# Kernel optimization log

Hardware: AMD Instinct MI355X
Metric: run time of the kernel (lower is better)

## Reference

```python
import jax, jax.numpy as jnp
import numpy as np

N, E, F_IN, HID, EPS = 50000, 800000, 128, 256, 1e-5

def _glorot(key, shape):
    scale = 1.0 / np.sqrt(shape[0])
    return jax.random.uniform(key, shape, jnp.float32, -scale, scale)

def setup_inputs() -> dict:
    key = jax.random.key(0)
    ks = jax.random.split(key, 20)
    x = jax.random.normal(ks[0], (N, F_IN), jnp.float32)
    edge_index = jax.random.randint(ks[1], (2, E), 0, N, jnp.int64)
    inp = {"x": x, "edge_index": edge_index}
    dims = [F_IN, HID, HID]
    for i in range(3):
        d_in = dims[i]
        inp[f"Wn{i}"] = _glorot(ks[2 + 4 * i], (d_in, HID))      # lin_l weight (neighbors), with bias
        inp[f"bn{i}"] = jnp.zeros((HID,), jnp.float32)
        inp[f"Wr{i}"] = _glorot(ks[3 + 4 * i], (d_in, HID))      # lin_r weight (root), no bias
        inp[f"g{i}"] = jnp.ones((HID,), jnp.float32)              # BN gamma
        inp[f"b{i}"] = jnp.zeros((HID,), jnp.float32)             # BN beta
    return inp

def _sage_bn_elu(x, src, dst, Wn, bn, Wr, g, b):
    # mean aggregation of source features onto destination nodes
    agg = jax.ops.segment_sum(x[src], dst, num_segments=N)                      # [N, d_in]
    deg = jax.ops.segment_sum(jnp.ones((src.shape[0],), x.dtype), dst, num_segments=N)
    agg = agg / jnp.maximum(deg, 1.0)[:, None]
    h = agg @ Wn + bn + x @ Wr                                                  # SAGEConv(root_weight=True)
    mu = jnp.mean(h, axis=0)
    var = jnp.mean((h - mu) ** 2, axis=0)                                       # biased var (BN training)
    h = (h - mu) * jax.lax.rsqrt(var + EPS) * g + b
    return jnp.where(h > 0, h, jnp.expm1(h))                                    # ELU(alpha=1)

def reference(x, edge_index, Wn0, bn0, Wr0, g0, b0, Wn1, bn1, Wr1, g1, b1, Wn2, bn2, Wr2, g2, b2):
    src, dst = edge_index[0], edge_index[1]
    h = _sage_bn_elu(x, src, dst, Wn0, bn0, Wr0, g0, b0)
    h = _sage_bn_elu(h, src, dst, Wn1, bn1, Wr1, g1, b1)
    h = _sage_bn_elu(h, src, dst, Wn2, bn2, Wr2, g2, b2)
    return h
```

## Files before the change

### kernel.cpp

```cpp
#include <hip/hip_runtime.h>
#include <math.h>

#define N_NODES 50000
#define N_EDGES 800000
#define F_IN    128
#define HID     256
#define BN_EPS  1e-5f
#define SCAN_BLOCKS ((N_NODES + 255) / 256)
#define RB256       ((N_NODES + 255) / 256)

typedef unsigned int uint;
typedef __attribute__((ext_vector_type(8))) short bf16x8;
typedef __attribute__((ext_vector_type(4))) float f32x4;

__device__ __forceinline__ float bf2f(unsigned short u) {
    return __uint_as_float((uint)u << 16);
}
__device__ __forceinline__ unsigned short f2bf(float f) {
    uint u = __float_as_uint(f);
    return (unsigned short)((u + 0x7FFFu + ((u >> 16) & 1u)) >> 16);
}

__device__ __forceinline__ void gload16(const unsigned short* g, unsigned short* l) {
    __builtin_amdgcn_global_load_lds(
        (const __attribute__((address_space(1))) void*)g,
        (__attribute__((address_space(3))) void*)l, 16, 0, 0);
}

__device__ __forceinline__ void acc_u4(float* a, uint4 v) {
    a[0] += bf2f((unsigned short)(v.x & 0xFFFF)); a[1] += bf2f((unsigned short)(v.x >> 16));
    a[2] += bf2f((unsigned short)(v.y & 0xFFFF)); a[3] += bf2f((unsigned short)(v.y >> 16));
    a[4] += bf2f((unsigned short)(v.z & 0xFFFF)); a[5] += bf2f((unsigned short)(v.z >> 16));
    a[6] += bf2f((unsigned short)(v.w & 0xFFFF)); a[7] += bf2f((unsigned short)(v.w >> 16));
}
__device__ __forceinline__ void acc_u4m(float* a, uint4 v, float m) {
    a[0] += m * bf2f((unsigned short)(v.x & 0xFFFF)); a[1] += m * bf2f((unsigned short)(v.x >> 16));
    a[2] += m * bf2f((unsigned short)(v.y & 0xFFFF)); a[3] += m * bf2f((unsigned short)(v.y >> 16));
    a[4] += m * bf2f((unsigned short)(v.z & 0xFFFF)); a[5] += m * bf2f((unsigned short)(v.z >> 16));
    a[6] += m * bf2f((unsigned short)(v.w & 0xFFFF)); a[7] += m * bf2f((unsigned short)(v.w >> 16));
}

__global__ void hist_kernel(const int* __restrict__ dst, int* __restrict__ deg) {
    int e = blockIdx.x * blockDim.x + threadIdx.x;
    if (e < N_EDGES) atomicAdd(&deg[dst[e]], 1);
}

__global__ __launch_bounds__(256) void scan1_kernel(const int* __restrict__ deg,
                                                    int* __restrict__ row_ptr,
                                                    int* __restrict__ partials) {
    __shared__ int sm[256];
    int i = blockIdx.x * 256 + threadIdx.x;
    int v = (i < N_NODES) ? deg[i] : 0;
    sm[threadIdx.x] = v;
    __syncthreads();
    for (int off = 1; off < 256; off <<= 1) {
        int t = (threadIdx.x >= off) ? sm[threadIdx.x - off] : 0;
        __syncthreads();
        sm[threadIdx.x] += t;
        __syncthreads();
    }
    if (i < N_NODES) row_ptr[i] = sm[threadIdx.x] - v;
    if (threadIdx.x == 255) partials[blockIdx.x] = sm[255];
}

__global__ __launch_bounds__(256) void scan2_kernel(int* __restrict__ partials) {
    __shared__ int sm[256];
    int t = threadIdx.x;
    int v = (t < SCAN_BLOCKS) ? partials[t] : 0;
    sm[t] = v;
    __syncthreads();
    for (int off = 1; off < 256; off <<= 1) {
        int p = (t >= off) ? sm[t - off] : 0;
        __syncthreads();
        sm[t] += p;
        __syncthreads();
    }
    if (t < SCAN_BLOCKS) partials[t] = sm[t] - v;
}

__global__ __launch_bounds__(256) void scan3_kernel(int* __restrict__ row_ptr,
                                                    int* __restrict__ cursor,
                                                    const int* __restrict__ partials) {
    int i = blockIdx.x * 256 + threadIdx.x;
    if (i < N_NODES) {
        int v = row_ptr[i] + partials[blockIdx.x];
        row_ptr[i] = v;
        cursor[i]  = v;
    }
    if (i == 0) row_ptr[N_NODES] = N_EDGES;
}

__global__ void fill_kernel(const int* __restrict__ src, const int* __restrict__ dst,
                            int* __restrict__ cursor, int* __restrict__ csr_src) {
    int e = blockIdx.x * blockDim.x + threadIdx.x;
    if (e >= N_EDGES) return;
    int pos = atomicAdd(&cursor[dst[e]], 1);
    csr_src[pos] = src[e];
}

__global__ void cast_bf16_kernel(const float* __restrict__ x, unsigned short* __restrict__ xb,
                                 int total4) {
    int i = blockIdx.x * blockDim.x + threadIdx.x;
    if (i >= total4) return;
    float4 v = *(const float4*)&x[(long)i * 4];
    unsigned short o[4] = {f2bf(v.x), f2bf(v.y), f2bf(v.z), f2bf(v.w)};
    *(uint2*)&xb[(long)i * 4] = *(const uint2*)o;
}

__global__ __launch_bounds__(256) void wt_kernel(const float* __restrict__ Wn,
                                                 const float* __restrict__ Wr,
                                                 int K1, int KT, unsigned short* __restrict__ WT) {
    int n  = threadIdx.x;
    int k0 = blockIdx.x * 16;
    unsigned short o[16];
#pragma unroll
    for (int j = 0; j < 16; ++j) {
        int k = k0 + j;
        float v = (k < K1) ? Wn[k * HID + n] : Wr[(k - K1) * HID + n];
        o[j] = f2bf(v);
    }
    *(uint4*)&WT[(long)n * KT + k0]     = *(const uint4*)&o[0];
    *(uint4*)&WT[(long)n * KT + k0 + 8] = *(const uint4*)&o[8];
}

template<int D>
__global__ __launch_bounds__(256) void gather_mean_kernel(
    const unsigned short* __restrict__ x, const int* __restrict__ row_ptr,
    const int* __restrict__ csr_src, unsigned short* __restrict__ agg) {
    int node = blockIdx.x * 4 + (threadIdx.x >> 6);
    int lane = threadIdx.x & 63;
    if (node >= N_NODES) return;
    int beg = row_ptr[node], end = row_ptr[node + 1];
    float acc[8];
#pragma unroll
    for (int j = 0; j < 8; j++) acc[j] = 0.f;
    int e = beg;

    if constexpr (D == 256) {
        const int half = lane >> 5;
        const long lo  = (long)(lane & 31) * 8;
        for (; e + 8 <= end; e += 8) {
            int s0 = csr_src[e + half],     s1 = csr_src[e + 2 + half];
            int s2 = csr_src[e + 4 + half], s3 = csr_src[e + 6 + half];
            uint4 v0 = *(const uint4*)&x[(long)s0 * 256 + lo];
            uint4 v1 = *(const uint4*)&x[(long)s1 * 256 + lo];
            uint4 v2 = *(const uint4*)&x[(long)s2 * 256 + lo];
            uint4 v3 = *(const uint4*)&x[(long)s3 * 256 + lo];
            acc_u4(acc, v0); acc_u4(acc, v1); acc_u4(acc, v2); acc_u4(acc, v3);
        }
        for (; e + 2 <= end; e += 2) {
            int s0 = csr_src[e + half];
            uint4 v0 = *(const uint4*)&x[(long)s0 * 256 + lo];
            acc_u4(acc, v0);
        }
        if (e < end) {
            int s0 = csr_src[e];
            uint4 v0 = *(const uint4*)&x[(long)s0 * 256 + lo];
            acc_u4m(acc, v0, (half == 0) ? 1.f : 0.f);
        }
#pragma unroll
        for (int j = 0; j < 8; j++) acc[j] += __shfl_xor(acc[j], 32);
        float inv = 1.0f / fmaxf((float)(end - beg), 1.0f);
        if (half == 0) {
            unsigned short ov[8];
#pragma unroll
            for (int j = 0; j < 8; j++) ov[j] = f2bf(acc[j] * inv);
            *(uint4*)&agg[(long)node * 256 + lo] = *(const uint4*)ov;
        }
    } else {
        const int grp = lane >> 4;
        const long lo = (long)(lane & 15) * 8;
        for (; e + 8 <= end; e += 8) {
            int sA = csr_src[e + grp], sB = csr_src[e + 4 + grp];
            uint4 vA = *(const uint4*)&x[(long)sA * 128 + lo];
            uint4 vB = *(const uint4*)&x[(long)sB * 128 + lo];
            acc_u4(acc, vA); acc_u4(acc, vB);
        }
        for (; e + 4 <= end; e += 4) {
            int sA = csr_src[e + grp];
            uint4 vA = *(const uint4*)&x[(long)sA * 128 + lo];
            acc_u4(acc, vA);
        }
        for (; e < end; e++) {
            int s0 = csr_src[e];
            uint4 v0 = *(const uint4*)&x[(long)s0 * 128 + lo];
            acc_u4m(acc, v0, (grp == 0) ? 1.f : 0.f);
        }
#pragma unroll
        for (int j = 0; j < 8; j++) {
            acc[j] += __shfl_xor(acc[j], 32);
            acc[j] += __shfl_xor(acc[j], 16);
        }
        float inv = 1.0f / fmaxf((float)(end - beg), 1.0f);
        if (lane < 16) {
            unsigned short ov[8];
#pragma unroll
            for (int j = 0; j < 8; j++) ov[j] = f2bf(acc[j] * inv);
            *(uint4*)&agg[(long)node * 128 + lo] = *(const uint4*)ov;
        }
    }
}

template<int K1, int K2>
__global__ __launch_bounds__(512) void mfma_gemm_kernel(
    const unsigned short* __restrict__ A1, const unsigned short* __restrict__ A2,
    const unsigned short* __restrict__ WT, const float* __restrict__ bias,
    unsigned short* __restrict__ Hout, float* __restrict__ sred) {
    constexpr int KT = K1 + K2;
    constexpr int NITER = KT / 64;
    __shared__ unsigned short As[2][256 * 64];
    __shared__ unsigned short Bs[2][256 * 64];

    const int tid  = threadIdx.x;
    const int wave = tid >> 6;
    const int lane = tid & 63;
    const int m16  = lane & 15;
    const int quad = lane >> 4;
    const int WR   = wave >> 2;
    const int WC   = wave & 3;
    const int r0   = blockIdx.x * 256;
    const int rl = lane >> 3;
    const int cl = lane & 7;
    const int csw = cl ^ rl;

    f32x4 acc[8][4];
#pragma unroll
    for (int mt = 0; mt < 8; mt++)
#pragma unroll
        for (int nt = 0; nt < 4; nt++) acc[mt][nt] = (f32x4){0.f, 0.f, 0.f, 0.f};

    auto issue = [&](int t) {
        const int buf = t & 1;
        const int k0  = t * 64;
        const unsigned short* Ab;
        int pitch, kk;
        if (k0 < K1) { Ab = A1; pitch = K1; kk = k0; }
        else         { Ab = A2; pitch = K2; kk = k0 - K1; }
#pragma unroll
        for (int j = 0; j < 4; ++j) {
            int lr = wave * 32 + j * 8 + rl;
            long gr = min(r0 + lr, N_NODES - 1);
            gload16(&Ab[gr * pitch + kk + csw * 8], &As[buf][(wave * 32 + j * 8) * 64]);
        }
#pragma unroll
        for (int j = 0; j < 4; ++j) {
            long gn = wave * 32 + j * 8 + rl;
            gload16(&WT[gn * KT + k0 + csw * 8], &Bs[buf][(wave * 32 + j * 8) * 64]);
        }
    };

    issue(0);

#pragma unroll
    for (int it = 0; it < NITER; ++it) {
        const int cur = it & 1;
        if (it + 1 < NITER) {
            issue(it + 1);
            asm volatile("s_waitcnt vmcnt(8)" ::: "memory");
        } else {
            asm volatile("s_waitcnt vmcnt(0)" ::: "memory");
        }
        __builtin_amdgcn_s_barrier();
#pragma unroll
        for (int ks = 0; ks < 2; ++ks) {
            bf16x8 afrag[8], bfrag[4];
#pragma unroll
            for (int mt = 0; mt < 8; mt++) {
                int ar = WR * 128 + mt * 16 + m16;
                afrag[mt] = *(const bf16x8*)&As[cur][ar * 64 + (((ks * 4 + quad) ^ (m16 & 7)) * 8)];
            }
#pragma unroll
            for (int nt = 0; nt < 4; nt++) {
                int br = WC * 64 + nt * 16 + m16;
                bfrag[nt] = *(const bf16x8*)&Bs[cur][br * 64 + (((ks * 4 + quad) ^ (m16 & 7)) * 8)];
            }
#pragma unroll
            for (int mt = 0; mt < 8; mt++)
#pragma unroll
                for (int nt = 0; nt < 4; nt++)
                    acc[mt][nt] = __builtin_amdgcn_mfma_f32_16x16x32_bf16(
                        afrag[mt], bfrag[nt], acc[mt][nt], 0, 0, 0);
        }
        __builtin_amdgcn_s_barrier();
    }

#pragma unroll
    for (int nt = 0; nt < 4; nt++) {
        int lcol = WC * 64 + nt * 16 + m16;
        float bv = bias[lcol];
        float s = 0.f, q = 0.f;
#pragma unroll
        for (int mt = 0; mt < 8; mt++) {
#pragma unroll
            for (int reg = 0; reg < 4; reg++) {
                int row = r0 + WR * 128 + mt * 16 + quad * 4 + reg;
                float v = acc[mt][nt][reg] + bv;
                if (row < N_NODES) {
                    Hout[(long)row * HID + lcol] = f2bf(v);
                    s += v;
                    q += v * v;
                }
            }
        }
        s += __shfl_xor(s, 16); s += __shfl_xor(s, 32);
        q += __shfl_xor(q, 16); q += __shfl_xor(q, 32);
        if (quad == 0) {
            float* base = &sred[(long)(blockIdx.x * 2 + WR) * 512];
            base[lcol]       = s;
            base[256 + lcol] = q;
        }
    }
}

__global__ __launch_bounds__(512) void bn_reduce_kernel(const float* __restrict__ sred,
                                                        const float* __restrict__ g,
                                                        const float* __restrict__ b,
                                                        float* __restrict__ ss, int nrows) {
    __shared__ float qsm[256];
    int t  = threadIdx.x;
    int ch = t & 255;
    int off = (t < 256) ? 0 : 256;
    float S0 = 0.f, S1 = 0.f, S2 = 0.f, S3 = 0.f;
    int rb = 0;
    for (; rb + 4 <= nrows; rb += 4) {
        S0 += sred[(long)(rb + 0) * 512 + off + ch];
        S1 += sred[(long)(rb + 1) * 512 + off + ch];
        S2 += sred[(long)(rb + 2) * 512 + off + ch];
        S3 += sred[(long)(rb + 3) * 512 + off + ch];
    }
    for (; rb < nrows; rb++) S0 += sred[(long)rb * 512 + off + ch];
    float Sv = (S0 + S1) + (S2 + S3);
    if (t >= 256) qsm[ch] = Sv;
    __syncthreads();
    if (t < 256) {
        float mu  = Sv * (1.0f / N_NODES);
        float var = qsm[ch] * (1.0f / N_NODES) - mu * mu;
        var = fmaxf(var, 0.f);
        float sc = rsqrtf(var + BN_EPS) * g[ch];
        ss[ch]       = sc;
        ss[HID + ch] = b[ch] - mu * sc;
    }
}

template<bool OUT32>
__global__ void bn_elu_kernel(const unsigned short* __restrict__ h, const float* __restrict__ ss,
                              void* __restrict__ out) {
    const int total4 = N_NODES * HID / 4;
    int i = blockIdx.x * blockDim.x + threadIdx.x;
    if (i >= total4) return;
    int c4 = (i % (HID / 4)) * 4;
    uint2 v = *(const uint2*)&h[(long)i * 4];
    float4 sc = *(const float4*)&ss[c4];
    float4 sh = *(const float4*)&ss[HID + c4];
    float in[4] = {bf2f((unsigned short)(v.x & 0xFFFF)), bf2f((unsigned short)(v.x >> 16)),
                   bf2f((unsigned short)(v.y & 0xFFFF)), bf2f((unsigned short)(v.y >> 16))};
    float scv[4] = {sc.x, sc.y, sc.z, sc.w};
    float shv[4] = {sh.x, sh.y, sh.z, sh.w};
    float o[4];
#pragma unroll
    for (int j = 0; j < 4; j++) {
        float t = fmaf(in[j], scv[j], shv[j]);
        o[j] = t > 0.f ? t : expm1f(t);
    }
    if (OUT32) {
        float4 ov = {o[0], o[1], o[2], o[3]};
        *(float4*)&((float*)out)[(long)i * 4] = ov;
    } else {
        unsigned short ov[4] = {f2bf(o[0]), f2bf(o[1]), f2bf(o[2]), f2bf(o[3])};
        *(uint2*)&((unsigned short*)out)[(long)i * 4] = *(const uint2*)ov;
    }
}

extern "C" void kernel_launch(void* const* d_in, const int* in_sizes, int n_in,
                              void* d_out, int out_size, void* d_ws, size_t ws_size,
                              hipStream_t stream) {
    const float* x   = (const float*)d_in[0];
    const int*   ei  = (const int*)d_in[1];
    const int*   src = ei;
    const int*   dst = ei + N_EDGES;
    const float* Wn[3] = {(const float*)d_in[2],  (const float*)d_in[7],  (const float*)d_in[12]};
    const float* bn[3] = {(const float*)d_in[3],  (const float*)d_in[8],  (const float*)d_in[13]};
    const float* Wr[3] = {(const float*)d_in[4],  (const float*)d_in[9],  (const float*)d_in[14]};
    const float* g [3] = {(const float*)d_in[5],  (const float*)d_in[10], (const float*)d_in[15]};
    const float* b [3] = {(const float*)d_in[6],  (const float*)d_in[11], (const float*)d_in[16]};
    float* out = (float*)d_out;

    const size_t BF = (size_t)N_NODES * HID * 2;
    char* ws = (char*)d_ws;
    unsigned short* B0  = (unsigned short*)(ws);
    unsigned short* B1  = (unsigned short*)(ws + BF);
    unsigned short* B2  = (unsigned short*)(ws + 2 * BF);
    unsigned short* XB  = (unsigned short*)(ws + 3 * BF);
    char* ws2 = ws + 3 * BF + (size_t)N_NODES * F_IN * 2;
    unsigned short* WT0 = (unsigned short*)(ws2);
    unsigned short* WT1 = (unsigned short*)(ws2 + 256 * 256 * 2);
    unsigned short* WT2 = (unsigned short*)(ws2 + 256 * 256 * 2 + 256 * 512 * 2);
    char* ws3 = ws2 + 256 * 256 * 2 + 2 * (256 * 512 * 2);
    int*   row_ptr = (int*)ws3;
    int*   cursor  = row_ptr + (N_NODES + 1);
    int*   deg_i   = cursor + N_NODES;
    int*   partial = deg_i + N_NODES;
    int*   csr_src = partial + SCAN_BLOCKS;
    float* sred    = (float*)(csr_src + N_EDGES);
    float* ss      = sred + (size_t)2 * RB256 * 512;

    const int eb = (N_EDGES + 255) / 256;
    const int gather_blocks = (N_NODES + 3) / 4;
    const int elu_blocks = (N_NODES * HID / 4 + 255) / 256;

    hipMemsetAsync(deg_i, 0, N_NODES * sizeof(int), stream);
    hist_kernel<<<eb, 256, 0, stream>>>(dst, deg_i);
    scan1_kernel<<<SCAN_BLOCKS, 256, 0, stream>>>(deg_i, row_ptr, partial);
    scan2_kernel<<<1, 256, 0, stream>>>(partial);
    scan3_kernel<<<SCAN_BLOCKS, 256, 0, stream>>>(row_ptr, cursor, partial);
    fill_kernel<<<eb, 256, 0, stream>>>(src, dst, cursor, csr_src);
    cast_bf16_kernel<<<(N_NODES * F_IN / 4 + 255) / 256, 256, 0, stream>>>(x, XB, N_NODES * F_IN / 4);
    wt_kernel<<<(2 * F_IN) / 16, 256, 0, stream>>>(Wn[0], Wr[0], F_IN, 2 * F_IN, WT0);
    wt_kernel<<<(2 * HID) / 16, 256, 0, stream>>>(Wn[1], Wr[1], HID, 2 * HID, WT1);
    wt_kernel<<<(2 * HID) / 16, 256, 0, stream>>>(Wn[2], Wr[2], HID, 2 * HID, WT2);

    gather_mean_kernel<F_IN><<<gather_blocks, 256, 0, stream>>>(XB, row_ptr, csr_src, B0);
    mfma_gemm_kernel<F_IN, F_IN><<<RB256, 512, 0, stream>>>(B0, XB, WT0, bn[0], B1, sred);
    bn_reduce_kernel<<<1, 512, 0, stream>>>(sred, g[0], b[0], ss, 2 * RB256);
    bn_elu_kernel<false><<<elu_blocks, 256, 0, stream>>>(B1, ss, B2);

    gather_mean_kernel<HID><<<gather_blocks, 256, 0, stream>>>(B2, row_ptr, csr_src, B0);
    mfma_gemm_kernel<HID, HID><<<RB256, 512, 0, stream>>>(B0, B2, WT1, bn[1], B1, sred);
    bn_reduce_kernel<<<1, 512, 0, stream>>>(sred, g[1], b[1], ss, 2 * RB256);
    bn_elu_kernel<false><<<elu_blocks, 256, 0, stream>>>(B1, ss, B2);

    gather_mean_kernel<HID><<<gather_blocks, 256, 0, stream>>>(B2, row_ptr, csr_src, B0);
    mfma_gemm_kernel<HID, HID><<<RB256, 512, 0, stream>>>(B0, B2, WT2, bn[2], B1, sred);
    bn_reduce_kernel<<<1, 512, 0, stream>>>(sred, g[2], b[2], ss, 2 * RB256);
    bn_elu_kernel<true><<<elu_blocks, 256, 0, stream>>>(B1, ss, out);
}
```

Before: 578.0 us.

## Fuse prep kernels, rank-based CSR fill, fold BN reduce into GEMM tail

Merges the cast, memset and weight-transpose launches into one prep kernel. CSR construction now records each edge's atomic rank during the histogram and drops scan2 by having each scan3 block sum its preceding partials. The fill step then needs no atomics and uses nontemporal stores. The BN statistics reduction moves into the last GEMM block through a ticket counter, and the gather loops are unrolled deeper for more loads in flight. The aim is fewer launches and less serialization, at the cost of a serial tail block in each GEMM and more register pressure in the gather.

```diff
diff --git a/kernel.cpp b/kernel.cpp
--- a/kernel.cpp
+++ b/kernel.cpp
@@ -8,6 +8,8 @@
 #define BN_EPS  1e-5f
 #define SCAN_BLOCKS ((N_NODES + 255) / 256)
 #define RB256       ((N_NODES + 255) / 256)
+#define CAST_BLOCKS (N_NODES * F_IN / 4 / 256)
+#define WT_BLOCKS   (16 + 32 + 32)
 
 typedef unsigned int uint;
 typedef __attribute__((ext_vector_type(8))) short bf16x8;
@@ -40,9 +42,46 @@
     a[6] += m * bf2f((unsigned short)(v.w & 0xFFFF)); a[7] += m * bf2f((unsigned short)(v.w >> 16));
 }
 
-__global__ void hist_kernel(const int* __restrict__ dst, int* __restrict__ deg) {
+__global__ __launch_bounds__(256) void prep_kernel(
+    const float* __restrict__ x, unsigned short* __restrict__ xb,
+    const float* __restrict__ Wn0, const float* __restrict__ Wr0, unsigned short* __restrict__ WT0,
+    const float* __restrict__ Wn1, const float* __restrict__ Wr1, unsigned short* __restrict__ WT1,
+    const float* __restrict__ Wn2, const float* __restrict__ Wr2, unsigned short* __restrict__ WT2,
+    int* __restrict__ deg, int* __restrict__ tickets) {
+    int bb = blockIdx.x;
+    if (bb < CAST_BLOCKS) {
+        int i = bb * 256 + threadIdx.x;
+        float4 v = *(const float4*)&x[(long)i * 4];
+        unsigned short o[4] = {f2bf(v.x), f2bf(v.y), f2bf(v.z), f2bf(v.w)};
+        *(uint2*)&xb[(long)i * 4] = *(const uint2*)o;
+    } else if (bb < CAST_BLOCKS + SCAN_BLOCKS) {
+        int i = (bb - CAST_BLOCKS) * 256 + threadIdx.x;
+        if (i < N_NODES) deg[i] = 0;
+        if (bb == CAST_BLOCKS && threadIdx.x < 3) tickets[threadIdx.x] = 0;
+    } else {
+        int wb = bb - (CAST_BLOCKS + SCAN_BLOCKS);
+        const float* Wn; const float* Wr; unsigned short* WT; int K1, KT, kb;
+        if (wb < 16)      { Wn = Wn0; Wr = Wr0; WT = WT0; K1 = F_IN; KT = 2 * F_IN; kb = wb; }
+        else if (wb < 48) { Wn = Wn1; Wr = Wr1; WT = WT1; K1 = HID;  KT = 2 * HID;  kb = wb - 16; }
+        else              { Wn = Wn2; Wr = Wr2; WT = WT2; K1 = HID;  KT = 2 * HID;  kb = wb - 48; }
+        int n  = threadIdx.x;
+        int k0 = kb * 16;
+        unsigned short o[16];
+#pragma unroll
+        for (int j = 0; j < 16; ++j) {
+            int k = k0 + j;
+            float v = (k < K1) ? Wn[k * HID + n] : Wr[(k - K1) * HID + n];
+            o[j] = f2bf(v);
+        }
+        *(uint4*)&WT[(long)n * KT + k0]     = *(const uint4*)&o[0];
+        *(uint4*)&WT[(long)n * KT + k0 + 8] = *(const uint4*)&o[8];
+    }
+}
+
+__global__ void hist_kernel(const int* __restrict__ dst, int* __restrict__ deg,
+                            int* __restrict__ rank) {
     int e = blockIdx.x * blockDim.x + threadIdx.x;
-    if (e < N_EDGES) atomicAdd(&deg[dst[e]], 1);
+    if (e < N_EDGES) rank[e] = atomicAdd(&deg[dst[e]], 1);
 }
 
 __global__ __launch_bounds__(256) void scan1_kernel(const int* __restrict__ deg,
@@ -63,64 +102,28 @@
     if (threadIdx.x == 255) partials[blockIdx.x] = sm[255];
 }
 
-__global__ __launch_bounds__(256) void scan2_kernel(int* __restrict__ partials) {
-    __shared__ int sm[256];
+__global__ __launch_bounds__(256) void scan3_kernel(int* __restrict__ row_ptr,
+                                                    const int* __restrict__ partials) {
+    __shared__ int red[4];
     int t = threadIdx.x;
-    int v = (t < SCAN_BLOCKS) ? partials[t] : 0;
-    sm[t] = v;
+    int v = (t < SCAN_BLOCKS && t < (int)blockIdx.x) ? partials[t] : 0;
+#pragma unroll
+    for (int off = 32; off; off >>= 1) v += __shfl_down(v, off);
+    if ((t & 63) == 0) red[t >> 6] = v;
     __syncthreads();
-    for (int off = 1; off < 256; off <<= 1) {
-        int p = (t >= off) ? sm[t - off] : 0;
-        __syncthreads();
-        sm[t] += p;
-        __syncthreads();
-    }
-    if (t < SCAN_BLOCKS) partials[t] = sm[t] - v;
-}
-
-__global__ __launch_bounds__(256) void scan3_kernel(int* __restrict__ row_ptr,
-                                                    int* __restrict__ cursor,
-                                                    const int* __restrict__ partials) {
-    int i = blockIdx.x * 256 + threadIdx.x;
-    if (i < N_NODES) {
-        int v = row_ptr[i] + partials[blockIdx.x];
-        row_ptr[i] = v;
-        cursor[i]  = v;
-    }
+    int base = red[0] + red[1] + red[2] + red[3];
+    int i = blockIdx.x * 256 + t;
+    if (i < N_NODES) row_ptr[i] += base;
     if (i == 0) row_ptr[N_NODES] = N_EDGES;
 }
 
 __global__ void fill_kernel(const int* __restrict__ src, const int* __restrict__ dst,
-                            int* __restrict__ cursor, int* __restrict__ csr_src) {
+                            const int* __restrict__ rank, const int* __restrict__ row_ptr,
+                            int* __restrict__ csr_src) {
     int e = blockIdx.x * blockDim.x + threadIdx.x;
     if (e >= N_EDGES) return;
-    int pos = atomicAdd(&cursor[dst[e]], 1);
-    csr_src[pos] = src[e];
-}
-
-__global__ void cast_bf16_kernel(const float* __restrict__ x, unsigned short* __restrict__ xb,
-                                 int total4) {
-    int i = blockIdx.x * blockDim.x + threadIdx.x;
-    if (i >= total4) return;
-    float4 v = *(const float4*)&x[(long)i * 4];
-    unsigned short o[4] = {f2bf(v.x), f2bf(v.y), f2bf(v.z), f2bf(v.w)};
-    *(uint2*)&xb[(long)i * 4] = *(const uint2*)o;
-}
-
-__global__ __launch_bounds__(256) void wt_kernel(const float* __restrict__ Wn,
-                                                 const float* __restrict__ Wr,
-                                                 int K1, int KT, unsigned short* __restrict__ WT) {
-    int n  = threadIdx.x;
-    int k0 = blockIdx.x * 16;
-    unsigned short o[16];
-#pragma unroll
-    for (int j = 0; j < 16; ++j) {
-        int k = k0 + j;
-        float v = (k < K1) ? Wn[k * HID + n] : Wr[(k - K1) * HID + n];
-        o[j] = f2bf(v);
-    }
-    *(uint4*)&WT[(long)n * KT + k0]     = *(const uint4*)&o[0];
-    *(uint4*)&WT[(long)n * KT + k0 + 8] = *(const uint4*)&o[8];
+    int pos = row_ptr[dst[e]] + rank[e];
+    __builtin_nontemporal_store(src[e], &csr_src[pos]);
 }
 
 template<int D>
@@ -139,6 +142,22 @@
     if constexpr (D == 256) {
         const int half = lane >> 5;
         const long lo  = (long)(lane & 31) * 8;
+        for (; e + 16 <= end; e += 16) {
+            int s0 = csr_src[e + half],      s1 = csr_src[e + 2 + half];
+            int s2 = csr_src[e + 4 + half],  s3 = csr_src[e + 6 + half];
+            int s4 = csr_src[e + 8 + half],  s5 = csr_src[e + 10 + half];
+            int s6 = csr_src[e + 12 + half], s7 = csr_src[e + 14 + half];
+            uint4 v0 = *(const uint4*)&x[(long)s0 * 256 + lo];
+            uint4 v1 = *(const uint4*)&x[(long)s1 * 256 + lo];
+            uint4 v2 = *(const uint4*)&x[(long)s2 * 256 + lo];
+            uint4 v3 = *(const uint4*)&x[(long)s3 * 256 + lo];
+            uint4 v4 = *(const uint4*)&x[(long)s4 * 256 + lo];
+            uint4 v5 = *(const uint4*)&x[(long)s5 * 256 + lo];
+            uint4 v6 = *(const uint4*)&x[(long)s6 * 256 + lo];
+            uint4 v7 = *(const uint4*)&x[(long)s7 * 256 + lo];
+            acc_u4(acc, v0); acc_u4(acc, v1); acc_u4(acc, v2); acc_u4(acc, v3);
+            acc_u4(acc, v4); acc_u4(acc, v5); acc_u4(acc, v6); acc_u4(acc, v7);
+        }
         for (; e + 8 <= end; e += 8) {
             int s0 = csr_src[e + half],     s1 = csr_src[e + 2 + half];
             int s2 = csr_src[e + 4 + half], s3 = csr_src[e + 6 + half];
@@ -170,6 +189,15 @@
     } else {
         const int grp = lane >> 4;
         const long lo = (long)(lane & 15) * 8;
+        for (; e + 16 <= end; e += 16) {
+            int sA = csr_src[e + grp],     sB = csr_src[e + 4 + grp];
+            int sC = csr_src[e + 8 + grp], sD = csr_src[e + 12 + grp];
+            uint4 vA = *(const uint4*)&x[(long)sA * 128 + lo];
+            uint4 vB = *(const uint4*)&x[(long)sB * 128 + lo];
+            uint4 vC = *(const uint4*)&x[(long)sC * 128 + lo];
+            uint4 vD = *(const uint4*)&x[(long)sD * 128 + lo];
+            acc_u4(acc, vA); acc_u4(acc, vB); acc_u4(acc, vC); acc_u4(acc, vD);
+        }
         for (; e + 8 <= end; e += 8) {
             int sA = csr_src[e + grp], sB = csr_src[e + 4 + grp];
             uint4 vA = *(const uint4*)&x[(long)sA * 128 + lo];
@@ -205,11 +233,16 @@
 __global__ __launch_bounds__(512) void mfma_gemm_kernel(
     const unsigned short* __restrict__ A1, const unsigned short* __restrict__ A2,
     const unsigned short* __restrict__ WT, const float* __restrict__ bias,
-    unsigned short* __restrict__ Hout, float* __restrict__ sred) {
+    const float* __restrict__ gam, const float* __restrict__ bet,
+    unsigned short* __restrict__ Hout, float* __restrict__ sred,
+    float* __restrict__ ss, int* __restrict__ ticket) {
     constexpr int KT = K1 + K2;
     constexpr int NITER = KT / 64;
+    constexpr int NROWS = 2 * RB256;
     __shared__ unsigned short As[2][256 * 64];
     __shared__ unsigned short Bs[2][256 * 64];
+    __shared__ float qsm[256];
+    __shared__ int lastflag;
 
     const int tid  = threadIdx.x;
     const int wave = tid >> 6;
@@ -310,35 +343,35 @@
             base[256 + lcol] = q;
         }
     }
-}
-
-__global__ __launch_bounds__(512) void bn_reduce_kernel(const float* __restrict__ sred,
-                                                        const float* __restrict__ g,
-                                                        const float* __restrict__ b,
-                                                        float* __restrict__ ss, int nrows) {
-    __shared__ float qsm[256];
-    int t  = threadIdx.x;
-    int ch = t & 255;
-    int off = (t < 256) ? 0 : 256;
-    float S0 = 0.f, S1 = 0.f, S2 = 0.f, S3 = 0.f;
-    int rb = 0;
-    for (; rb + 4 <= nrows; rb += 4) {
-        S0 += sred[(long)(rb + 0) * 512 + off + ch];
-        S1 += sred[(long)(rb + 1) * 512 + off + ch];
-        S2 += sred[(long)(rb + 2) * 512 + off + ch];
-        S3 += sred[(long)(rb + 3) * 512 + off + ch];
-    }
-    for (; rb < nrows; rb++) S0 += sred[(long)rb * 512 + off + ch];
-    float Sv = (S0 + S1) + (S2 + S3);
-    if (t >= 256) qsm[ch] = Sv;
+
+    __threadfence();
     __syncthreads();
-    if (t < 256) {
-        float mu  = Sv * (1.0f / N_NODES);
-        float var = qsm[ch] * (1.0f / N_NODES) - mu * mu;
-        var = fmaxf(var, 0.f);
-        float sc = rsqrtf(var + BN_EPS) * g[ch];
-        ss[ch]       = sc;
-        ss[HID + ch] = b[ch] - mu * sc;
+    if (tid == 0) lastflag = (atomicAdd(ticket, 1) == (int)gridDim.x - 1) ? 1 : 0;
+    __syncthreads();
+    if (!lastflag) return;
+    __threadfence();
+    {
+        int off = (tid < 256) ? 0 : 256;
+        int ch  = tid & 255;
+        float S0 = 0.f, S1 = 0.f, S2 = 0.f, S3 = 0.f;
+#pragma unroll 1
+        for (int rb = 0; rb < NROWS; rb += 4) {
+            S0 += sred[(long)(rb + 0) * 512 + off + ch];
+            S1 += sred[(long)(rb + 1) * 512 + off + ch];
+            S2 += sred[(long)(rb + 2) * 512 + off + ch];
+            S3 += sred[(long)(rb + 3) * 512 + off + ch];
+        }
+        float Sv = (S0 + S1) + (S2 + S3);
+        if (tid >= 256) qsm[ch] = Sv;
+        __syncthreads();
+        if (tid < 256) {
+            float mu  = Sv * (1.0f / N_NODES);
+            float var = qsm[ch] * (1.0f / N_NODES) - mu * mu;
+            var = fmaxf(var, 0.f);
+            float sc = rsqrtf(var + BN_EPS) * gam[ch];
+            ss[ch]       = sc;
+            ss[HID + ch] = bet[ch] - mu * sc;
+        }
     }
 }
 
@@ -397,40 +430,38 @@
     unsigned short* WT2 = (unsigned short*)(ws2 + 256 * 256 * 2 + 256 * 512 * 2);
     char* ws3 = ws2 + 256 * 256 * 2 + 2 * (256 * 512 * 2);
     int*   row_ptr = (int*)ws3;
-    int*   cursor  = row_ptr + (N_NODES + 1);
-    int*   deg_i   = cursor + N_NODES;
+    int*   deg_i   = row_ptr + (N_NODES + 1);
     int*   partial = deg_i + N_NODES;
-    int*   csr_src = partial + SCAN_BLOCKS;
-    float* sred    = (float*)(csr_src + N_EDGES);
+    int*   rank    = partial + SCAN_BLOCKS;
+    int*   csr_src = rank + N_EDGES;
+    int*   tickets = csr_src + N_EDGES;
+    float* sred    = (float*)(tickets + 4);
     float* ss      = sred + (size_t)2 * RB256 * 512;
 
     const int eb = (N_EDGES + 255) / 256;
     const int gather_blocks = (N_NODES + 3) / 4;
     const int elu_blocks = (N_NODES * HID / 4 + 255) / 256;
-
-    hipMemsetAsync(deg_i, 0, N_NODES * sizeof(int), stream);
-    hist_kernel<<<eb, 256, 0, stream>>>(dst, deg_i);
+    const int prep_blocks = CAST_BLOCKS + SCAN_BLOCKS + WT_BLOCKS;
+
+    prep_kernel<<<prep_blocks, 256, 0, stream>>>(x, XB,
+        Wn[0], Wr[0], WT0, Wn[1], Wr[1], WT1, Wn[2], Wr[2], WT2, deg_i, tickets);
+    hist_kernel<<<eb, 256, 0, stream>>>(dst, deg_i, rank);
     scan1_kernel<<<SCAN_BLOCKS, 256, 0, stream>>>(deg_i, row_ptr, partial);
-    scan2_kernel<<<1, 256, 0, stream>>>(partial);
-    scan3_kernel<<<SCAN_BLOCKS, 256, 0, stream>>>(row_ptr, cursor, partial);
-    fill_kernel<<<eb, 256, 0, stream>>>(src, dst, cursor, csr_src);
-    cast_bf16_kernel<<<(N_NODES * F_IN / 4 + 255) / 256, 256, 0, stream>>>(x, XB, N_NODES * F_IN / 4);
-    wt_kernel<<<(2 * F_IN) / 16, 256, 0, stream>>>(Wn[0], Wr[0], F_IN, 2 * F_IN, WT0);
-    wt_kernel<<<(2 * HID) / 16, 256, 0, stream>>>(Wn[1], Wr[1], HID, 2 * HID, WT1);
-    wt_kernel<<<(2 * HID) / 16, 256, 0, stream>>>(Wn[2], Wr[2], HID, 2 * HID, WT2);
+    scan3_kernel<<<SCAN_BLOCKS, 256, 0, stream>>>(row_ptr, partial);
+    fill_kernel<<<eb, 256, 0, stream>>>(src, dst, rank, row_ptr, csr_src);
 
     gather_mean_kernel<F_IN><<<gather_blocks, 256, 0, stream>>>(XB, row_ptr, csr_src, B0);
-    mfma_gemm_kernel<F_IN, F_IN><<<RB256, 512, 0, stream>>>(B0, XB, WT0, bn[0], B1, sred);
-    bn_reduce_kernel<<<1, 512, 0, stream>>>(sred, g[0], b[0], ss, 2 * RB256);
+    mfma_gemm_kernel<F_IN, F_IN><<<RB256, 512, 0, stream>>>(B0, XB, WT0, bn[0], g[0], b[0],
+                                                            B1, sred, ss, &tickets[0]);
     bn_elu_kernel<false><<<elu_blocks, 256, 0, stream>>>(B1, ss, B2);
 
     gather_mean_kernel<HID><<<gather_blocks, 256, 0, stream>>>(B2, row_ptr, csr_src, B0);
-    mfma_gemm_kernel<HID, HID><<<RB256, 512, 0, stream>>>(B0, B2, WT1, bn[1], B1, sred);
-    bn_reduce_kernel<<<1, 512, 0, stream>>>(sred, g[1], b[1], ss, 2 * RB256);
+    mfma_gemm_kernel<HID, HID><<<RB256, 512, 0, stream>>>(B0, B2, WT1, bn[1], g[1], b[1],
+                                                          B1, sred, ss, &tickets[1]);
     bn_elu_kernel<false><<<elu_blocks, 256, 0, stream>>>(B1, ss, B2);
 
     gather_mean_kernel<HID><<<gather_blocks, 256, 0, stream>>>(B2, row_ptr, csr_src, B0);
-    mfma_gemm_kernel<HID, HID><<<RB256, 512, 0, stream>>>(B0, B2, WT2, bn[2], B1, sred);
-    bn_reduce_kernel<<<1, 512, 0, stream>>>(sred, g[2], b[2], ss, 2 * RB256);
+    mfma_gemm_kernel<HID, HID><<<RB256, 512, 0, stream>>>(B0, B2, WT2, bn[2], g[2], b[2],
+                                                          B1, sred, ss, &tickets[2]);
     bn_elu_kernel<true><<<elu_blocks, 256, 0, stream>>>(B1, ss, out);
 }
```

New measurement: 662.6 us. 1.15x slower.
